# Kernel tuning notes

Hardware: AMD Instinct MI355X
Metric: run time of the kernel (lower is better)

## Reference

```python
import jax, jax.numpy as jnp
import numpy as np

NODE_DIM = 256
EDGE_DIM = 128
HEADS = 8
HEAD_DIM = 32
HIDDEN = HEADS * HEAD_DIM  # 256
B, N = 2, 768
LN_EPS = 1e-5


def _layernorm(x, w, b):
    mu = jnp.mean(x, axis=-1, keepdims=True)
    var = jnp.mean(jnp.square(x - mu), axis=-1, keepdims=True)
    return (x - mu) * jax.lax.rsqrt(var + LN_EPS) * w + b


def setup_inputs() -> dict:
    key = jax.random.key(0)
    ks = jax.random.split(key, 10)
    s_node = NODE_DIM ** -0.5
    s_edge = EDGE_DIM ** -0.5
    s_hid = HIDDEN ** -0.5
    return {
        "node": jax.random.normal(ks[0], (B, N, NODE_DIM), jnp.float32),
        "edge": jax.random.normal(ks[1], (B, N, N, EDGE_DIM), jnp.float32),
        "ln_node_w": jnp.ones((NODE_DIM,), jnp.float32),
        "ln_node_b": jnp.zeros((NODE_DIM,), jnp.float32),
        "ln_edge_w": jnp.ones((EDGE_DIM,), jnp.float32),
        "ln_edge_b": jnp.zeros((EDGE_DIM,), jnp.float32),
        "Wq": jax.random.normal(ks[2], (NODE_DIM, HIDDEN), jnp.float32) * s_node,
        "Wk": jax.random.normal(ks[3], (NODE_DIM, HIDDEN), jnp.float32) * s_node,
        "Wv": jax.random.normal(ks[4], (NODE_DIM, HIDDEN), jnp.float32) * s_node,
        "Wb": jax.random.normal(ks[5], (EDGE_DIM, HEADS), jnp.float32) * s_edge,
        "Wg": jax.random.normal(ks[6], (NODE_DIM, HIDDEN), jnp.float32) * s_node,
        "bg": jnp.zeros((HIDDEN,), jnp.float32),
        "Wo": jax.random.normal(ks[7], (HIDDEN, NODE_DIM), jnp.float32) * s_hid,
        "bo": jnp.zeros((NODE_DIM,), jnp.float32),
    }


def reference(node, edge, ln_node_w, ln_node_b, ln_edge_w, ln_edge_b,
              Wq, Wk, Wv, Wb, Wg, bg, Wo, bo):
    scale = HEAD_DIM ** -0.5
    x = _layernorm(node, ln_node_w, ln_node_b)          # [b, i, node_dim]
    y = _layernorm(edge, ln_edge_w, ln_edge_b)          # [b, i, j, edge_dim]

    def heads(t):  # [b, i, hidden] -> [b, h, i, d]
        b_, i_, _ = t.shape
        return t.reshape(b_, i_, HEADS, HEAD_DIM).transpose(0, 2, 1, 3)

    q = heads(x @ Wq)
    k = heads(x @ Wk)
    v = heads(x @ Wv)
    g = heads(jax.nn.sigmoid(x @ Wg + bg))
    bias = jnp.einsum('bije,eh->bhij', y, Wb)           # [b, h, i, j]

    logits = jnp.einsum('bhid,bhjd->bhij', q, k) * scale + bias
    attn = jax.nn.softmax(logits, axis=-1)
    res = jnp.einsum('bhij,bhjd->bhid', attn, v) * g    # gated values
    res = res.transpose(0, 2, 1, 3).reshape(node.shape[0], node.shape[1], HIDDEN)
    return res @ Wo + bo
```

## Files before the change

### kernel.cpp

```cpp
#include <hip/hip_runtime.h>
#include <hip/hip_bf16.h>
#include <math.h>

#define BN 1536
#define NN 768
#define SCALE 0.17677669529663687f
#define NROWS (BN * NN)

__device__ __forceinline__ float sel8(const float* a, int idx) {
    float r = a[0];
#pragma unroll
    for (int t = 1; t < 8; ++t) r = (idx == t) ? a[t] : r;
    return r;
}

__global__ __launch_bounds__(256) void k_lnproj(
    const float* __restrict__ node, const float* __restrict__ lnw,
    const float* __restrict__ lnb, const float* __restrict__ Wq,
    const float* __restrict__ Wk, const float* __restrict__ Wv,
    const float* __restrict__ Wg, const float* __restrict__ bg,
    float* __restrict__ q, float* __restrict__ k,
    float* __restrict__ v, float* __restrict__ g)
{
    __shared__ float xs[8][256];
    const int tid = threadIdx.x;
    const int wave = tid >> 6, lane = tid & 63;
    const int row0 = blockIdx.x * 8;

#pragma unroll
    for (int rr = 0; rr < 2; ++rr) {
        const int r = wave * 2 + rr;
        float4 xv = ((const float4*)node)[(size_t)(row0 + r) * 64 + lane];
        float s1 = xv.x + xv.y + xv.z + xv.w;
        float s2 = fmaf(xv.x, xv.x, fmaf(xv.y, xv.y, fmaf(xv.z, xv.z, xv.w * xv.w)));
#pragma unroll
        for (int off = 32; off > 0; off >>= 1) {
            s1 += __shfl_xor(s1, off);
            s2 += __shfl_xor(s2, off);
        }
        const float mu = s1 * (1.f / 256.f);
        const float rstd = rsqrtf(s2 * (1.f / 256.f) - mu * mu + 1e-5f);
        float4 w4 = ((const float4*)lnw)[lane];
        float4 b4 = ((const float4*)lnb)[lane];
        xs[r][lane * 4 + 0] = (xv.x - mu) * rstd * w4.x + b4.x;
        xs[r][lane * 4 + 1] = (xv.y - mu) * rstd * w4.y + b4.y;
        xs[r][lane * 4 + 2] = (xv.z - mu) * rstd * w4.z + b4.z;
        xs[r][lane * 4 + 3] = (xv.w - mu) * rstd * w4.w + b4.w;
    }
    __syncthreads();

    float aq[8] = {}, ak[8] = {}, av[8] = {}, ag[8] = {};
    for (int e4 = 0; e4 < 64; ++e4) {
        const int e = e4 * 4;
        float wq_[4], wk_[4], wv_[4], wg_[4];
#pragma unroll
        for (int t = 0; t < 4; ++t) {
            wq_[t] = Wq[(e + t) * 256 + tid];
            wk_[t] = Wk[(e + t) * 256 + tid];
            wv_[t] = Wv[(e + t) * 256 + tid];
            wg_[t] = Wg[(e + t) * 256 + tid];
        }
#pragma unroll
        for (int r = 0; r < 8; ++r) {
            float4 xr = *(const float4*)&xs[r][e];
            aq[r] = fmaf(xr.x, wq_[0], fmaf(xr.y, wq_[1], fmaf(xr.z, wq_[2], fmaf(xr.w, wq_[3], aq[r]))));
            ak[r] = fmaf(xr.x, wk_[0], fmaf(xr.y, wk_[1], fmaf(xr.z, wk_[2], fmaf(xr.w, wk_[3], ak[r]))));
            av[r] = fmaf(xr.x, wv_[0], fmaf(xr.y, wv_[1], fmaf(xr.z, wv_[2], fmaf(xr.w, wv_[3], av[r]))));
            ag[r] = fmaf(xr.x, wg_[0], fmaf(xr.y, wg_[1], fmaf(xr.z, wg_[2], fmaf(xr.w, wg_[3], ag[r]))));
        }
    }
    const float bgv = bg[tid];
#pragma unroll
    for (int r = 0; r < 8; ++r) {
        const size_t o = (size_t)(row0 + r) * 256 + tid;
        q[o] = aq[r] * SCALE;
        k[o] = ak[r];
        v[o] = av[r];
        g[o] = 1.f / (1.f + __expf(-(ag[r] + bgv)));
    }
}

__global__ __launch_bounds__(256) void k_bias(
    const float* __restrict__ edge, const float* __restrict__ lnw,
    const float* __restrict__ lnb, const float* __restrict__ Wb,
    float* __restrict__ bias)
{
    const int tid = threadIdx.x;
    const int gl = tid & 15;

    float wbf[8][8];
    float c1p[8], c0p[8];
#pragma unroll
    for (int hh = 0; hh < 8; ++hh) { c1p[hh] = 0.f; c0p[hh] = 0.f; }
#pragma unroll
    for (int t = 0; t < 8; ++t) {
        const int c = gl * 8 + t;
        const float w = lnw[c], bb = lnb[c];
#pragma unroll
        for (int hh = 0; hh < 8; ++hh) {
            const float wb_ = Wb[c * 8 + hh];
            wbf[t][hh] = w * wb_;
            c1p[hh] += wbf[t][hh];
            c0p[hh] = fmaf(bb, wb_, c0p[hh]);
        }
    }
#pragma unroll
    for (int off = 1; off < 16; off <<= 1) {
#pragma unroll
        for (int hh = 0; hh < 8; ++hh) {
            c1p[hh] += __shfl_xor(c1p[hh], off);
            c0p[hh] += __shfl_xor(c0p[hh], off);
        }
    }
    const float c1s = sel8(c1p, gl & 7);
    const float c0s = sel8(c0p, gl & 7);

    const int stride = gridDim.x * 16;
    for (int r = blockIdx.x * 16 + (tid >> 4); r < NROWS; r += stride) {
        const float4 e0 = ((const float4*)edge)[(size_t)r * 32 + gl * 2];
        const float4 e1 = ((const float4*)edge)[(size_t)r * 32 + gl * 2 + 1];
        float s1 = (e0.x + e0.y) + (e0.z + e0.w) + ((e1.x + e1.y) + (e1.z + e1.w));
        float s2 = fmaf(e0.x, e0.x, fmaf(e0.y, e0.y, fmaf(e0.z, e0.z, e0.w * e0.w)));
        s2 = fmaf(e1.x, e1.x, fmaf(e1.y, e1.y, fmaf(e1.z, e1.z, fmaf(e1.w, e1.w, s2))));
        float d[8];
#pragma unroll
        for (int hh = 0; hh < 8; ++hh) {
            float t0 = e0.x * wbf[0][hh];
            t0 = fmaf(e0.y, wbf[1][hh], t0);
            t0 = fmaf(e0.z, wbf[2][hh], t0);
            t0 = fmaf(e0.w, wbf[3][hh], t0);
            t0 = fmaf(e1.x, wbf[4][hh], t0);
            t0 = fmaf(e1.y, wbf[5][hh], t0);
            t0 = fmaf(e1.z, wbf[6][hh], t0);
            t0 = fmaf(e1.w, wbf[7][hh], t0);
            d[hh] = t0;
        }
#pragma unroll
        for (int off = 1; off < 16; off <<= 1) {
            s1 += __shfl_xor(s1, off);
            s2 += __shfl_xor(s2, off);
#pragma unroll
            for (int hh = 0; hh < 8; ++hh) d[hh] += __shfl_xor(d[hh], off);
        }
        if (gl < 8) {
            const float mu = s1 * (1.f / 128.f);
            const float rstd = rsqrtf(s2 * (1.f / 128.f) - mu * mu + 1e-5f);
            const float dh = sel8(d, gl);
            bias[(size_t)r * 8 + gl] = rstd * (dh - mu * c1s) + c0s;
        }
    }
}

__global__ __launch_bounds__(256) void k_attn2(
    const float* __restrict__ bias,
    const float* __restrict__ q, const float* __restrict__ k,
    const float* __restrict__ v, const float* __restrict__ g,
    float* __restrict__ res)
{
    __shared__ float mrg[4][64][6];
    const int tid = threadIdx.x;
    const int wave = tid >> 6, lane = tid & 63;
    const int bi = blockIdx.x;
    const int b = bi / NN;
    const int h = lane >> 3;

    const float4 q4 = ((const float4*)q)[(size_t)bi * 64 + lane];
    const float* brow = bias + (size_t)bi * NN * 8;
    const size_t kb = (size_t)b * NN * 64;

    float m = -3e38f, s = 0.f;
    float4 acc = make_float4(0.f, 0.f, 0.f, 0.f);

    for (int jp = wave * 2; jp < NN; jp += 8) {
        const int j0 = jp, j1 = jp + 1;
        const float4 k0 = ((const float4*)k)[kb + (size_t)j0 * 64 + lane];
        const float4 k1 = ((const float4*)k)[kb + (size_t)j1 * 64 + lane];
        const float b0 = brow[j0 * 8 + h];
        const float b1 = brow[j1 * 8 + h];
        const float4 v0 = ((const float4*)v)[kb + (size_t)j0 * 64 + lane];
        const float4 v1 = ((const float4*)v)[kb + (size_t)j1 * 64 + lane];

        float d0 = fmaf(q4.x, k0.x, fmaf(q4.y, k0.y, fmaf(q4.z, k0.z, q4.w * k0.w)));
        float d1 = fmaf(q4.x, k1.x, fmaf(q4.y, k1.y, fmaf(q4.z, k1.z, q4.w * k1.w)));
        d0 += __shfl_xor(d0, 1); d1 += __shfl_xor(d1, 1);
        d0 += __shfl_xor(d0, 2); d1 += __shfl_xor(d1, 2);
        d0 += __shfl_xor(d0, 4); d1 += __shfl_xor(d1, 4);
        const float l0 = d0 + b0;
        const float l1 = d1 + b1;

        const float mn = fmaxf(m, fmaxf(l0, l1));
        const float sc = __expf(m - mn);
        const float p0 = __expf(l0 - mn);
        const float p1 = __expf(l1 - mn);
        s = fmaf(s, sc, p0 + p1);
        m = mn;
        acc.x = fmaf(p1, v1.x, fmaf(p0, v0.x, acc.x * sc));
        acc.y = fmaf(p1, v1.y, fmaf(p0, v0.y, acc.y * sc));
        acc.z = fmaf(p1, v1.z, fmaf(p0, v0.z, acc.z * sc));
        acc.w = fmaf(p1, v1.w, fmaf(p0, v0.w, acc.w * sc));
    }

    mrg[wave][lane][0] = m;
    mrg[wave][lane][1] = s;
    mrg[wave][lane][2] = acc.x;
    mrg[wave][lane][3] = acc.y;
    mrg[wave][lane][4] = acc.z;
    mrg[wave][lane][5] = acc.w;
    __syncthreads();
    if (wave == 0) {
        float M = mrg[0][lane][0];
#pragma unroll
        for (int w2 = 1; w2 < 4; ++w2) M = fmaxf(M, mrg[w2][lane][0]);
        float S = 0.f;
        float4 A = make_float4(0.f, 0.f, 0.f, 0.f);
#pragma unroll
        for (int w2 = 0; w2 < 4; ++w2) {
            const float sc = __expf(mrg[w2][lane][0] - M);
            S = fmaf(mrg[w2][lane][1], sc, S);
            A.x = fmaf(mrg[w2][lane][2], sc, A.x);
            A.y = fmaf(mrg[w2][lane][3], sc, A.y);
            A.z = fmaf(mrg[w2][lane][4], sc, A.z);
            A.w = fmaf(mrg[w2][lane][5], sc, A.w);
        }
        const float4 g4 = ((const float4*)g)[(size_t)bi * 64 + lane];
        const float inv = 1.f / S;
        float4 r;
        r.x = A.x * inv * g4.x;
        r.y = A.y * inv * g4.y;
        r.z = A.z * inv * g4.z;
        r.w = A.w * inv * g4.w;
        ((float4*)res)[(size_t)bi * 64 + lane] = r;
    }
}

__global__ __launch_bounds__(256) void k_outproj(
    const float* __restrict__ res, const float* __restrict__ Wo,
    const float* __restrict__ bo, float* __restrict__ out)
{
    __shared__ float xs[8][256];
    const int tid = threadIdx.x;
    const int row0 = blockIdx.x * 8;

#pragma unroll
    for (int t = tid; t < 512; t += 256)
        ((float4*)&xs[0][0])[t] = ((const float4*)(res + (size_t)row0 * 256))[t];
    __syncthreads();

    float a[8] = {};
    for (int e4 = 0; e4 < 64; ++e4) {
        const int e = e4 * 4;
        float w_[4];
#pragma unroll
        for (int t = 0; t < 4; ++t) w_[t] = Wo[(e + t) * 256 + tid];
#pragma unroll
        for (int r = 0; r < 8; ++r) {
            float4 xr = *(const float4*)&xs[r][e];
            a[r] = fmaf(xr.x, w_[0], fmaf(xr.y, w_[1], fmaf(xr.z, w_[2], fmaf(xr.w, w_[3], a[r]))));
        }
    }
    const float bov = bo[tid];
#pragma unroll
    for (int r = 0; r < 8; ++r)
        out[(size_t)(row0 + r) * 256 + tid] = a[r] + bov;
}

extern "C" void kernel_launch(void* const* d_in, const int* in_sizes, int n_in,
                              void* d_out, int out_size, void* d_ws, size_t ws_size,
                              hipStream_t stream) {
    const float* node = (const float*)d_in[0];
    const float* edge = (const float*)d_in[1];
    const float* lnnw = (const float*)d_in[2];
    const float* lnnb = (const float*)d_in[3];
    const float* lnew = (const float*)d_in[4];
    const float* lneb = (const float*)d_in[5];
    const float* Wq   = (const float*)d_in[6];
    const float* Wk   = (const float*)d_in[7];
    const float* Wv   = (const float*)d_in[8];
    const float* Wb   = (const float*)d_in[9];
    const float* Wg   = (const float*)d_in[10];
    const float* bg   = (const float*)d_in[11];
    const float* Wo   = (const float*)d_in[12];
    const float* bo   = (const float*)d_in[13];
    float* out = (float*)d_out;

    float* ws = (float*)d_ws;
    const size_t NT = (size_t)BN * 256;
    float* q    = ws;
    float* k    = ws + NT;
    float* v    = ws + 2 * NT;
    float* g    = ws + 3 * NT;
    float* res  = ws + 4 * NT;
    float* bias = ws + 5 * NT;

    k_lnproj<<<BN / 8, 256, 0, stream>>>(node, lnnw, lnnb, Wq, Wk, Wv, Wg, bg, q, k, v, g);
    k_bias<<<2048, 256, 0, stream>>>(edge, lnew, lneb, Wb, bias);
    k_attn2<<<BN, 256, 0, stream>>>(bias, q, k, v, g, res);
    k_outproj<<<BN / 8, 256, 0, stream>>>(res, Wo, bo, out);
}
```

Measured before the change: 405.3 us.

## Double-buffer edge rows into LDS via async global_load_lds in bias kernel

Restructures the edge-LayerNorm/bias projection kernel so each wave owns a contiguous chunk of rows and streams 16-row tiles into double-buffered, XOR-swizzled LDS using direct global-to-LDS loads, overlapping the next tile's fetch with compute on the current one. Each row is now handled by 8 lanes with 16 channels each, which cuts shuffle-reduction steps, and the grid shrinks to 256 blocks. The aim is to keep the edge stream (the dominant memory traffic) saturating bandwidth. The trade-offs are more registers for the 16x8 weight slice, fewer resident waves, and reliance on manual vmcnt waits being correct.

```diff
diff --git a/kernel.cpp b/kernel.cpp
--- a/kernel.cpp
+++ b/kernel.cpp
@@ -6,12 +6,22 @@
 #define NN 768
 #define SCALE 0.17677669529663687f
 #define NROWS (BN * NN)
+#define TROWS 16
+#define WAVES_TOTAL 1024
+#define ROWS_PER_WAVE (NROWS / WAVES_TOTAL)
+#define NTILES (ROWS_PER_WAVE / TROWS)
 
 __device__ __forceinline__ float sel8(const float* a, int idx) {
     float r = a[0];
 #pragma unroll
     for (int t = 1; t < 8; ++t) r = (idx == t) ? a[t] : r;
     return r;
+}
+
+__device__ __forceinline__ void gl_lds16(const float* g, float* l) {
+    __builtin_amdgcn_global_load_lds(
+        (const __attribute__((address_space(1))) void*)g,
+        (__attribute__((address_space(3))) void*)l, 16, 0, 0);
 }
 
 __global__ __launch_bounds__(256) void k_lnproj(
@@ -85,70 +95,131 @@
     const float* __restrict__ lnb, const float* __restrict__ Wb,
     float* __restrict__ bias)
 {
+    __shared__ float lds[4][2][TROWS * 128];
     const int tid = threadIdx.x;
-    const int gl = tid & 15;
-
-    float wbf[8][8];
+    const int wave = tid >> 6, lane = tid & 63;
+    const int g = lane & 7;
+
+    float wbf[16][8];
     float c1p[8], c0p[8];
 #pragma unroll
     for (int hh = 0; hh < 8; ++hh) { c1p[hh] = 0.f; c0p[hh] = 0.f; }
 #pragma unroll
-    for (int t = 0; t < 8; ++t) {
-        const int c = gl * 8 + t;
+    for (int cc = 0; cc < 16; ++cc) {
+        const int c = g * 16 + cc;
         const float w = lnw[c], bb = lnb[c];
-#pragma unroll
-        for (int hh = 0; hh < 8; ++hh) {
-            const float wb_ = Wb[c * 8 + hh];
-            wbf[t][hh] = w * wb_;
-            c1p[hh] += wbf[t][hh];
-            c0p[hh] = fmaf(bb, wb_, c0p[hh]);
-        }
-    }
-#pragma unroll
-    for (int off = 1; off < 16; off <<= 1) {
+        const float4 wa = ((const float4*)Wb)[c * 2];
+        const float4 wc = ((const float4*)Wb)[c * 2 + 1];
+        wbf[cc][0] = w * wa.x; wbf[cc][1] = w * wa.y;
+        wbf[cc][2] = w * wa.z; wbf[cc][3] = w * wa.w;
+        wbf[cc][4] = w * wc.x; wbf[cc][5] = w * wc.y;
+        wbf[cc][6] = w * wc.z; wbf[cc][7] = w * wc.w;
+        c0p[0] = fmaf(bb, wa.x, c0p[0]); c0p[1] = fmaf(bb, wa.y, c0p[1]);
+        c0p[2] = fmaf(bb, wa.z, c0p[2]); c0p[3] = fmaf(bb, wa.w, c0p[3]);
+        c0p[4] = fmaf(bb, wc.x, c0p[4]); c0p[5] = fmaf(bb, wc.y, c0p[5]);
+        c0p[6] = fmaf(bb, wc.z, c0p[6]); c0p[7] = fmaf(bb, wc.w, c0p[7]);
+#pragma unroll
+        for (int hh = 0; hh < 8; ++hh) c1p[hh] += wbf[cc][hh];
+    }
+#pragma unroll
+    for (int off = 1; off < 8; off <<= 1) {
 #pragma unroll
         for (int hh = 0; hh < 8; ++hh) {
             c1p[hh] += __shfl_xor(c1p[hh], off);
             c0p[hh] += __shfl_xor(c0p[hh], off);
         }
     }
-    const float c1s = sel8(c1p, gl & 7);
-    const float c0s = sel8(c0p, gl & 7);
-
-    const int stride = gridDim.x * 16;
-    for (int r = blockIdx.x * 16 + (tid >> 4); r < NROWS; r += stride) {
-        const float4 e0 = ((const float4*)edge)[(size_t)r * 32 + gl * 2];
-        const float4 e1 = ((const float4*)edge)[(size_t)r * 32 + gl * 2 + 1];
-        float s1 = (e0.x + e0.y) + (e0.z + e0.w) + ((e1.x + e1.y) + (e1.z + e1.w));
-        float s2 = fmaf(e0.x, e0.x, fmaf(e0.y, e0.y, fmaf(e0.z, e0.z, e0.w * e0.w)));
-        s2 = fmaf(e1.x, e1.x, fmaf(e1.y, e1.y, fmaf(e1.z, e1.z, fmaf(e1.w, e1.w, s2))));
-        float d[8];
-#pragma unroll
-        for (int hh = 0; hh < 8; ++hh) {
-            float t0 = e0.x * wbf[0][hh];
-            t0 = fmaf(e0.y, wbf[1][hh], t0);
-            t0 = fmaf(e0.z, wbf[2][hh], t0);
-            t0 = fmaf(e0.w, wbf[3][hh], t0);
-            t0 = fmaf(e1.x, wbf[4][hh], t0);
-            t0 = fmaf(e1.y, wbf[5][hh], t0);
-            t0 = fmaf(e1.z, wbf[6][hh], t0);
-            t0 = fmaf(e1.w, wbf[7][hh], t0);
-            d[hh] = t0;
-        }
-#pragma unroll
-        for (int off = 1; off < 16; off <<= 1) {
-            s1 += __shfl_xor(s1, off);
-            s2 += __shfl_xor(s2, off);
-#pragma unroll
-            for (int hh = 0; hh < 8; ++hh) d[hh] += __shfl_xor(d[hh], off);
-        }
-        if (gl < 8) {
+    const float c1s = sel8(c1p, g);
+    const float c0s = sel8(c0p, g);
+
+    const int wid = blockIdx.x * 4 + wave;
+    const size_t row0 = (size_t)wid * ROWS_PER_WAVE;
+    float* buf0 = &lds[wave][0][0];
+    float* buf1 = &lds[wave][1][0];
+
+    const int lh = lane >> 5;
+    const int u = lane & 31;
+#define PREFETCH(GBASE, BUF)                                              \
+    {                                                                     \
+        const float* _gb = (GBASE);                                       \
+        float* _lb = (BUF);                                               \
+        _Pragma("unroll")                                                 \
+        for (int _i = 0; _i < 8; ++_i) {                                  \
+            const int _r = 2 * _i + lh;                                   \
+            gl_lds16(_gb + _r * 128 + ((u ^ (_r & 7)) << 2),              \
+                     _lb + _i * 256);                                     \
+        }                                                                 \
+    }
+
+    PREFETCH(edge + row0 * 128, buf0);
+    float* cur = buf0;
+    float* nxt = buf1;
+
+    const int rgrp = lane >> 3;
+
+    for (int t = 0; t < NTILES; ++t) {
+        if (t + 1 < NTILES) {
+            PREFETCH(edge + (row0 + (size_t)(t + 1) * TROWS) * 128, nxt);
+            asm volatile("s_waitcnt vmcnt(8)" ::: "memory");
+        } else {
+            asm volatile("s_waitcnt vmcnt(0)" ::: "memory");
+        }
+        __builtin_amdgcn_sched_barrier(0);
+
+#pragma unroll
+        for (int p = 0; p < 2; ++p) {
+            const int rl = p * 8 + rgrp;
+            const int sw = rl & 7;
+            const float* rowb = cur + rl * 128;
+            const float4 x0 = *(const float4*)(rowb + (((g * 4 + 0) ^ sw) << 2));
+            const float4 x1 = *(const float4*)(rowb + (((g * 4 + 1) ^ sw) << 2));
+            const float4 x2 = *(const float4*)(rowb + (((g * 4 + 2) ^ sw) << 2));
+            const float4 x3 = *(const float4*)(rowb + (((g * 4 + 3) ^ sw) << 2));
+
+            float s1 = ((x0.x + x0.y) + (x0.z + x0.w)) + ((x1.x + x1.y) + (x1.z + x1.w))
+                     + ((x2.x + x2.y) + (x2.z + x2.w)) + ((x3.x + x3.y) + (x3.z + x3.w));
+            float s2 = fmaf(x0.x, x0.x, fmaf(x0.y, x0.y, fmaf(x0.z, x0.z, x0.w * x0.w)));
+            s2 = fmaf(x1.x, x1.x, fmaf(x1.y, x1.y, fmaf(x1.z, x1.z, fmaf(x1.w, x1.w, s2))));
+            s2 = fmaf(x2.x, x2.x, fmaf(x2.y, x2.y, fmaf(x2.z, x2.z, fmaf(x2.w, x2.w, s2))));
+            s2 = fmaf(x3.x, x3.x, fmaf(x3.y, x3.y, fmaf(x3.z, x3.z, fmaf(x3.w, x3.w, s2))));
+
+            float d[8];
+#pragma unroll
+            for (int hh = 0; hh < 8; ++hh) {
+                float a = x0.x * wbf[0][hh];
+                a = fmaf(x0.y, wbf[1][hh], a);
+                a = fmaf(x0.z, wbf[2][hh], a);
+                a = fmaf(x0.w, wbf[3][hh], a);
+                a = fmaf(x1.x, wbf[4][hh], a);
+                a = fmaf(x1.y, wbf[5][hh], a);
+                a = fmaf(x1.z, wbf[6][hh], a);
+                a = fmaf(x1.w, wbf[7][hh], a);
+                a = fmaf(x2.x, wbf[8][hh], a);
+                a = fmaf(x2.y, wbf[9][hh], a);
+                a = fmaf(x2.z, wbf[10][hh], a);
+                a = fmaf(x2.w, wbf[11][hh], a);
+                a = fmaf(x3.x, wbf[12][hh], a);
+                a = fmaf(x3.y, wbf[13][hh], a);
+                a = fmaf(x3.z, wbf[14][hh], a);
+                a = fmaf(x3.w, wbf[15][hh], a);
+                d[hh] = a;
+            }
+#pragma unroll
+            for (int off = 1; off < 8; off <<= 1) {
+                s1 += __shfl_xor(s1, off);
+                s2 += __shfl_xor(s2, off);
+#pragma unroll
+                for (int hh = 0; hh < 8; ++hh) d[hh] += __shfl_xor(d[hh], off);
+            }
             const float mu = s1 * (1.f / 128.f);
             const float rstd = rsqrtf(s2 * (1.f / 128.f) - mu * mu + 1e-5f);
-            const float dh = sel8(d, gl);
-            bias[(size_t)r * 8 + gl] = rstd * (dh - mu * c1s) + c0s;
-        }
-    }
+            const float dg = sel8(d, g);
+            bias[(row0 + (size_t)t * TROWS + rl) * 8 + g] =
+                rstd * (dg - mu * c1s) + c0s;
+        }
+        float* tmp = cur; cur = nxt; nxt = tmp;
+    }
+#undef PREFETCH
 }
 
 __global__ __launch_bounds__(256) void k_attn2(
@@ -293,7 +364,7 @@
     float* bias = ws + 5 * NT;
 
     k_lnproj<<<BN / 8, 256, 0, stream>>>(node, lnnw, lnnb, Wq, Wk, Wv, Wg, bg, q, k, v, g);
-    k_bias<<<2048, 256, 0, stream>>>(edge, lnew, lneb, Wb, bias);
+    k_bias<<<256, 256, 0, stream>>>(edge, lnew, lneb, Wb, bias);
     k_attn2<<<BN, 256, 0, stream>>>(bias, q, k, v, g, res);
     k_outproj<<<BN / 8, 256, 0, stream>>>(res, Wo, bo, out);
 }
```

New measurement: 389.2 us. 1.04x faster.
